# Kernel tuning notes

Hardware: AMD Instinct MI355X
Metric: run time of the kernel (lower is better)

The kernel has to match this reference:

```python
import jax, jax.numpy as jnp
import numpy as np

# bitsandbytes NF4 codebook (16 levels)
NF4_CODE = jnp.array([
    -1.0, -0.6961928009986877, -0.5250730514526367, -0.39491748809814453,
    -0.28444138169288635, -0.18477343022823334, -0.09105003625154495, 0.0,
    0.07958029955625534, 0.16093020141124725, 0.24611230194568634,
    0.33791524171829224, 0.44070982933044434, 0.5626170039176941,
    0.7229568362236023, 1.0], dtype=jnp.float32)

L, D, KV, F, V = 2, 4096, 1024, 14336, 32000   # layers, d_model, kv_dim, ffn, vocab
H, HK, HD = 32, 8, 128                          # q heads, kv heads, head dim
B, S = 2, 1024
BLK = 64                                        # NF4 quant blocksize
ROPE_THETA = 500000.0
RMS_EPS = 1e-5


def _dequant(idx, absmax, shape):
    # idx: uint8 flat codes in [0,16); absmax: fp32 per-64-element block scale
    w = NF4_CODE[idx.astype(jnp.int32)]
    return (w.reshape(-1, BLK) * absmax[:, None]).reshape(shape)


def _rmsnorm(x, w):
    return x * jax.lax.rsqrt(jnp.mean(x * x, axis=-1, keepdims=True) + RMS_EPS) * w


def _rope(x, cos, sin):
    d2 = x.shape[-1] // 2
    x1, x2 = x[..., :d2], x[..., d2:]
    return jnp.concatenate([x1 * cos - x2 * sin, x2 * cos + x1 * sin], axis=-1)


def setup_inputs() -> dict:
    key = jax.random.key(0)
    ks = iter(jax.random.split(key, 64))

    def idx(n):
        return jax.random.randint(next(ks), (n,), 0, 16).astype(jnp.uint8)

    def amax(n):
        return jax.random.uniform(next(ks), (n // BLK,), minval=0.01, maxval=0.05)

    def qw(n):
        return (jnp.stack([idx(n) for _ in range(L)]),
                jnp.stack([amax(n) for _ in range(L)]))

    inp = {}
    inp["input_ids"] = jax.random.randint(next(ks), (B, S), 0, V, dtype=jnp.int32)
    inp["attention_mask"] = jnp.ones((B, S), dtype=jnp.int32)
    inp["embed"] = jax.random.normal(next(ks), (V, D), dtype=jnp.float32) * 0.02
    inp["q_idx"], inp["q_absmax"] = qw(D * D)
    inp["k_idx"], inp["k_absmax"] = qw(KV * D)
    inp["v_idx"], inp["v_absmax"] = qw(KV * D)
    inp["o_idx"], inp["o_absmax"] = qw(D * D)
    inp["gate_idx"], inp["gate_absmax"] = qw(F * D)
    inp["up_idx"], inp["up_absmax"] = qw(F * D)
    inp["down_idx"], inp["down_absmax"] = qw(D * F)
    inp["ln1_w"] = jnp.ones((L, D), dtype=jnp.float32)
    inp["ln2_w"] = jnp.ones((L, D), dtype=jnp.float32)
    inp["final_ln_w"] = jnp.ones((D,), dtype=jnp.float32)
    return inp


def reference(input_ids, attention_mask, embed,
              q_idx, q_absmax, k_idx, k_absmax, v_idx, v_absmax,
              o_idx, o_absmax, gate_idx, gate_absmax, up_idx, up_absmax,
              down_idx, down_absmax, ln1_w, ln2_w, final_ln_w):
    b, s = input_ids.shape
    h = embed[input_ids]                                  # [B,S,D]
    pos = jnp.arange(s, dtype=jnp.float32)
    inv = 1.0 / (ROPE_THETA ** (jnp.arange(0, HD, 2, dtype=jnp.float32) / HD))
    ang = pos[:, None] * inv[None, :]                     # [S,HD/2]
    cos = jnp.cos(ang)[None, :, None, :]
    sin = jnp.sin(ang)[None, :, None, :]
    causal = jnp.tril(jnp.ones((s, s), dtype=bool))
    mask = causal[None, None] & (attention_mask[:, None, None, :] > 0)  # [B,1,S,S]
    neg = jnp.finfo(h.dtype).min

    for l in range(L):
        x = _rmsnorm(h, ln1_w[l])
        q = x @ _dequant(q_idx[l], q_absmax[l], (D, D)).T
        k = x @ _dequant(k_idx[l], k_absmax[l], (KV, D)).T
        v = x @ _dequant(v_idx[l], v_absmax[l], (KV, D)).T
        q = _rope(q.reshape(b, s, H, HD), cos, sin)
        k = _rope(k.reshape(b, s, HK, HD), cos, sin)
        v = v.reshape(b, s, HK, HD)
        k = jnp.repeat(k, H // HK, axis=2)                # GQA expand
        v = jnp.repeat(v, H // HK, axis=2)
        scores = jnp.einsum('bqhd,bkhd->bhqk', q, k) / np.float32(np.sqrt(HD))
        scores = jnp.where(mask, scores, neg)
        attn = jax.nn.softmax(scores, axis=-1)
        ctx = jnp.einsum('bhqk,bkhd->bqhd', attn, v).reshape(b, s, D)
        h = h + ctx @ _dequant(o_idx[l], o_absmax[l], (D, D)).T
        x = _rmsnorm(h, ln2_w[l])
        g = x @ _dequant(gate_idx[l], gate_absmax[l], (F, D)).T
        u = x @ _dequant(up_idx[l], up_absmax[l], (F, D)).T
        h = h + (jax.nn.silu(g) * u) @ _dequant(down_idx[l], down_absmax[l], (D, F)).T

    h = _rmsnorm(h, final_ln_w)                           # last hidden state
    m = attention_mask.astype(h.dtype)[..., None]         # masked mean pool
    pooled = (h * m).sum(axis=1) / jnp.clip(m.sum(axis=1), 1e-9)
    return pooled
```

## Files before the change

### kernel.cpp

```cpp
#include <hip/hip_runtime.h>
#include <hip/hip_fp16.h>
#include <cstdint>
#include <cstddef>

#define B_  2
#define S_  1024
#define D_  4096
#define KV_ 1024
#define F_  14336
#define H_  32
#define HK_ 8
#define HD_ 128
#define M_  2048

typedef _Float16 f16;
typedef f16   f16x8 __attribute__((ext_vector_type(8)));
typedef f16   f16x4 __attribute__((ext_vector_type(4)));
typedef float f32x4 __attribute__((ext_vector_type(4)));
typedef unsigned u32x2 __attribute__((ext_vector_type(2)));
typedef unsigned u32x4 __attribute__((ext_vector_type(4)));
typedef int      i32x4 __attribute__((ext_vector_type(4)));

#define AS1(p) ((const __attribute__((address_space(1))) void*)(p))
#define AS3(p) ((__attribute__((address_space(3))) void*)(p))

__device__ __constant__ float NF4_C[16] = {
 -1.0f, -0.6961928009986877f, -0.5250730514526367f, -0.39491748809814453f,
 -0.28444138169288635f, -0.18477343022823334f, -0.09105003625154495f, 0.0f,
 0.07958029955625534f, 0.16093020141124725f, 0.24611230194568634f,
 0.33791524171829224f, 0.44070982933044434f, 0.5626170039176941f,
 0.7229568362236023f, 1.0f };

#define WC_LAYER  218103808ull
#define WC_O      25165824ull
#define WC_G      41943040ull
#define WC_U      100663296ull
#define WC_D      159383552ull

__global__ void k_detect(const unsigned* __restrict__ p, int* __restrict__ flag){
    if (threadIdx.x == 0){
        int u8 = 0;
        for (int i = 0; i < 256; ++i) if (p[i] >= 16u) { u8 = 1; break; }
        *flag = u8;
    }
}

__global__ __launch_bounds__(256) void k_dequant_all(
        const void* __restrict__ qi, const void* __restrict__ ki, const void* __restrict__ vi,
        const void* __restrict__ oi, const void* __restrict__ gi, const void* __restrict__ ui,
        const void* __restrict__ di,
        const float* __restrict__ qa, const float* __restrict__ ka, const float* __restrict__ va,
        const float* __restrict__ oa, const float* __restrict__ ga, const float* __restrict__ ua,
        const float* __restrict__ da,
        f16* __restrict__ wc, const int* __restrict__ flag)
{
    __shared__ __half2 T[3856];
    int t = threadIdx.x;
    if (t < 256){
        int b0 = t & 15, b1 = t >> 4;
        T[b0 + (b1 << 8)] = __halves2half2(__float2half(NF4_C[b0]), __float2half(NF4_C[b1]));
    }
    __syncthreads();
    int blk = blockIdx.x;
    int l = blk / 106496; blk -= l * 106496;
    const size_t DDc = (size_t)D_ * D_, KVDc = (size_t)KV_ * D_, FDc = (size_t)F_ * D_;
    size_t oDD = (size_t)l * DDc, oKVD = (size_t)l * KVDc, oFD = (size_t)l * FDc;
    f16* wl = wc + (size_t)l * WC_LAYER;
    const void* src; const float* am; size_t so; f16* dst;
    if (blk < 8192)       { src = qi; am = qa; so = oDD;  dst = wl; }
    else if (blk < 10240) { src = ki; am = ka; so = oKVD; dst = wl + DDc;        blk -= 8192; }
    else if (blk < 12288) { src = vi; am = va; so = oKVD; dst = wl + DDc + KVDc; blk -= 10240; }
    else if (blk < 20480) { src = oi; am = oa; so = oDD;  dst = wl + WC_O;       blk -= 12288; }
    else if (blk < 49152) { src = gi; am = ga; so = oFD;  dst = wl + WC_G;       blk -= 20480; }
    else if (blk < 77824) { src = ui; am = ua; so = oFD;  dst = wl + WC_U;       blk -= 49152; }
    else                  { src = di; am = da; so = oFD;  dst = wl + WC_D;       blk -= 77824; }
    size_t i = ((size_t)blk * 256 + t) * 8;
    float amv = am[(so + i) >> 6];
    __half2 am2 = __float2half2_rn(amv);
    union { __half2 h2[4]; u32x4 u4; } R;
    if (*flag){
        u32x2 u = __builtin_nontemporal_load((const u32x2*)((const uint8_t*)src + so + i));
        R.h2[0] = __hmul2(T[u.x & 0xFFFFu], am2);
        R.h2[1] = __hmul2(T[u.x >> 16],     am2);
        R.h2[2] = __hmul2(T[u.y & 0xFFFFu], am2);
        R.h2[3] = __hmul2(T[u.y >> 16],     am2);
    } else {
        const i32x4* s4 = (const i32x4*)((const int*)src + so + i);
        i32x4 a0 = __builtin_nontemporal_load(s4);
        i32x4 a1 = __builtin_nontemporal_load(s4 + 1);
        R.h2[0] = __hmul2(T[a0.x | (a0.y << 8)], am2);
        R.h2[1] = __hmul2(T[a0.z | (a0.w << 8)], am2);
        R.h2[2] = __hmul2(T[a1.x | (a1.y << 8)], am2);
        R.h2[3] = __hmul2(T[a1.z | (a1.w << 8)], am2);
    }
    __builtin_nontemporal_store(R.u4, (u32x4*)(dst + i));
}

__global__ __launch_bounds__(256) void k_embed(const int* __restrict__ ids,
        const float* __restrict__ E, float* __restrict__ Hh)
{
    int row = blockIdx.x, t = threadIdx.x;
    int id = ids[row];
    const float4* s4 = (const float4*)(E + (size_t)id * D_);
    float4* d4 = (float4*)(Hh + (size_t)row * D_);
    #pragma unroll
    for (int i = 0; i < 4; ++i) d4[t + 256*i] = s4[t + 256*i];
}

__global__ __launch_bounds__(256) void k_ropetab(float* __restrict__ cosT, float* __restrict__ sinT){
    int id = blockIdx.x * 256 + threadIdx.x;
    int d = id & 63, s = id >> 6;
    float inv = powf(500000.0f, -(float)d * (1.0f/64.0f));
    float ang = (float)s * inv;
    cosT[id] = cosf(ang);
    sinT[id] = sinf(ang);
}

__global__ void k_maskadd(const int* __restrict__ am, float* __restrict__ ma){
    int i = blockIdx.x * 256 + threadIdx.x;
    ma[i] = am[i] ? 0.f : -1e30f;
}

template<int F16OUT>
__global__ __launch_bounds__(256) void k_rmsnorm(const float* __restrict__ X,
        const float* __restrict__ W, void* __restrict__ outv)
{
    int row = blockIdx.x, t = threadIdx.x;
    const float4* x4 = (const float4*)(X + (size_t)row * D_);
    float4 xs[4]; float ss = 0.f;
    #pragma unroll
    for (int i = 0; i < 4; ++i){
        xs[i] = x4[t + 256*i];
        ss += xs[i].x*xs[i].x + xs[i].y*xs[i].y + xs[i].z*xs[i].z + xs[i].w*xs[i].w;
    }
    for (int m = 32; m; m >>= 1) ss += __shfl_xor(ss, m, 64);
    __shared__ float red[4];
    if ((t & 63) == 0) red[t >> 6] = ss;
    __syncthreads();
    ss = red[0] + red[1] + red[2] + red[3];
    float rs = rsqrtf(ss * (1.0f / D_) + 1e-5f);
    #pragma unroll
    for (int i = 0; i < 4; ++i){
        int c0 = (t + 256*i) * 4;
        float4 wv = *(const float4*)(W + c0);
        float o0 = xs[i].x*rs*wv.x, o1 = xs[i].y*rs*wv.y;
        float o2 = xs[i].z*rs*wv.z, o3 = xs[i].w*rs*wv.w;
        if (F16OUT){
            f16x4 ov = { (f16)o0, (f16)o1, (f16)o2, (f16)o3 };
            *(f16x4*)((f16*)outv + (size_t)row * D_ + c0) = ov;
        } else {
            float4 ov = {o0, o1, o2, o3};
            *(float4*)((float*)outv + (size_t)row * D_ + c0) = ov;
        }
    }
}

template<int F16OUT>
__global__ __launch_bounds__(256) void k_combnorm(float* __restrict__ H,
        const float* __restrict__ p0, const float* __restrict__ p1,
        const float* __restrict__ W, void* __restrict__ outv)
{
    int row = blockIdx.x, t = threadIdx.x;
    size_t base = (size_t)row * D_;
    float4 xs[4]; float ss = 0.f;
    #pragma unroll
    for (int i = 0; i < 4; ++i){
        int c4 = (t + 256*i) * 4;
        float4 hv = *(const float4*)(H + base + c4);
        float4 a  = *(const float4*)(p0 + base + c4);
        float4 b  = *(const float4*)(p1 + base + c4);
        hv.x += a.x + b.x; hv.y += a.y + b.y; hv.z += a.z + b.z; hv.w += a.w + b.w;
        *(float4*)(H + base + c4) = hv;
        xs[i] = hv;
        ss += hv.x*hv.x + hv.y*hv.y + hv.z*hv.z + hv.w*hv.w;
    }
    for (int m = 32; m; m >>= 1) ss += __shfl_xor(ss, m, 64);
    __shared__ float red[4];
    if ((t & 63) == 0) red[t >> 6] = ss;
    __syncthreads();
    ss = red[0] + red[1] + red[2] + red[3];
    float rs = rsqrtf(ss * (1.0f / D_) + 1e-5f);
    #pragma unroll
    for (int i = 0; i < 4; ++i){
        int c0 = (t + 256*i) * 4;
        float4 wv = *(const float4*)(W + c0);
        float o0 = xs[i].x*rs*wv.x, o1 = xs[i].y*rs*wv.y;
        float o2 = xs[i].z*rs*wv.z, o3 = xs[i].w*rs*wv.w;
        if (F16OUT){
            f16x4 ov = { (f16)o0, (f16)o1, (f16)o2, (f16)o3 };
            *(f16x4*)((f16*)outv + base + c0) = ov;
        } else {
            float4 ov = {o0, o1, o2, o3};
            *(float4*)((float*)outv + base + c0) = ov;
        }
    }
}

__global__ __launch_bounds__(256) void k_qkvprep(const f16* __restrict__ qkv,
        f16* __restrict__ qr, f16* __restrict__ kr, f16* __restrict__ vtr,
        const float* __restrict__ cosT, const float* __restrict__ sinT)
{
    const int istr = D_ + 2 * KV_;
    int blk = blockIdx.x;
    if (blk < 16384){
        int p = blk * 256 + threadIdx.x;
        int d = p & 63;
        int h = (p >> 6) & 31;
        int s = (p >> 11) & (S_ - 1);
        int b = p >> 21;
        size_t ib = (size_t)(b * S_ + s) * istr + (size_t)h * HD_;
        float x1 = (float)qkv[ib + d], x2 = (float)qkv[ib + 64 + d];
        float c = cosT[s*64 + d], sn = sinT[s*64 + d];
        size_t ob = (((size_t)((b << 5) + h)) * S_ + (size_t)s) * HD_;
        qr[ob + d]      = (f16)(x1 * c - x2 * sn);
        qr[ob + 64 + d] = (f16)(x2 * c + x1 * sn);
    } else if (blk < 20480){
        int p = (blk - 16384) * 256 + threadIdx.x;
        int d = p & 63;
        int h = (p >> 6) & 7;
        int s = (p >> 9) & (S_ - 1);
        int b = p >> 19;
        size_t ib = (size_t)(b * S_ + s) * istr + (size_t)(D_) + (size_t)h * HD_;
        float x1 = (float)qkv[ib + d], x2 = (float)qkv[ib + 64 + d];
        float c = cosT[s*64 + d], sn = sinT[s*64 + d];
        size_t ob = (((size_t)((b << 3) + h)) * S_ + (size_t)s) * HD_;
        kr[ob + d]      = (f16)(x1 * c - x2 * sn);
        kr[ob + 64 + d] = (f16)(x2 * c + x1 * sn);
    } else {
        int p = (blk - 20480) * 256 + threadIdx.x;
        int s  = p & (S_ - 1);
        int d  = (p >> 10) & (HD_ - 1);
        int hk = (p >> 17) & (HK_ - 1);
        int b  = p >> 20;
        f16 v = qkv[(size_t)(b * S_ + s) * istr + (size_t)(D_ + KV_) + (size_t)hk * HD_ + d];
        vtr[(((size_t)(b * HK_ + hk)) * HD_ + d) * S_ + s] = v;
    }
}

__global__ __launch_bounds__(256) void k_flash(const f16* __restrict__ Qr, const f16* __restrict__ Kr,
        const f16* __restrict__ Vt, const float* __restrict__ mAddG, f16* __restrict__ ctx)
{
    __shared__ f16 KS[8192];
    __shared__ f16 VS[8192];
    __shared__ f16 PS[8192];
    const int t = threadIdx.x;
    const int w = t >> 6, l = t & 63;
    const int lr = l & 15, lg = l >> 4;
    const int qt = blockIdx.x, bh = blockIdx.y;
    const int b = bh >> 5, hh = bh & 31, hk = hh >> 2;
    const f16* Qb = Qr + ((size_t)bh * S_ + (size_t)qt*128) * HD_;
    const f16* Kb = Kr + (size_t)(b * HK_ + hk) * S_ * HD_;
    const f16* Vb = Vt + (size_t)(b * HK_ + hk) * HD_ * S_;

    auto stage16x128 = [&](const f16* src, int lds_, f16* dst){
        int rowl = t >> 4;
        int cs = ((t & 15) ^ (rowl & 7)) << 3;
        #pragma unroll
        for (int g = 0; g < 4; ++g)
            __builtin_amdgcn_global_load_lds(AS1(src + (size_t)(g*16 + rowl)*lds_ + cs),
                AS3(dst + g*2048 + w*512), 16, 0, 0);
    };
    auto stage32x64 = [&](const f16* src, int lds_, f16* dst){
        int rowl = t >> 3;
        int cs = ((t & 7) ^ (rowl & 7)) << 3;
        #pragma unroll
        for (int g = 0; g < 4; ++g)
            __builtin_amdgcn_global_load_lds(AS1(src + (size_t)(g*32 + rowl)*lds_ + cs),
                AS3(dst + g*2048 + w*512), 16, 0, 0);
    };

    stage16x128(Qb, HD_, KS);
    stage16x128(Qb + 64*HD_, HD_, VS);
    __syncthreads();
    f16x8 qF[2][4];
    {
        const f16* qsrc = (w < 2) ? KS : VS;
        int rbase = (w & 1) * 32;
        #pragma unroll
        for (int m = 0; m < 2; ++m)
            #pragma unroll
            for (int kd = 0; kd < 4; ++kd){
                int row = rbase + m*16 + lr;
                qF[m][kd] = *(const f16x8*)&qsrc[row*128 + (((kd*4 + lg) ^ (row & 7)) << 3)];
            }
    }
    __syncthreads();

    float mrow[2][4], lrow[2][4];
    f32x4 oacc[2][8];
    #pragma unroll
    for (int m = 0; m < 2; ++m)
        #pragma unroll
        for (int r = 0; r < 4; ++r){ mrow[m][r] = -1e30f; lrow[m][r] = 0.f; }
    #pragma unroll
    for (int m = 0; m < 2; ++m)
        #pragma unroll
        for (int dn = 0; dn < 8; ++dn){ f32x4 z = {0,0,0,0}; oacc[m][dn] = z; }

    const float ISQ = 0.08838834764831845f;
    const int ktMax = 2*qt + 1;

    for (int kt = 0; kt <= ktMax; ++kt){
        stage16x128(Kb + (size_t)(kt*64)*HD_, HD_, KS);
        __syncthreads();

        f32x4 sacc[2][4];
        #pragma unroll
        for (int m = 0; m < 2; ++m)
            #pragma unroll
            for (int n = 0; n < 4; ++n){ f32x4 z = {0,0,0,0}; sacc[m][n] = z; }
        #pragma unroll
        for (int n = 0; n < 4; ++n){
            int krow = n*16 + lr;
            #pragma unroll
            for (int kd = 0; kd < 4; ++kd){
                f16x8 kF = *(const f16x8*)&KS[krow*128 + (((kd*4 + lg) ^ (krow & 7)) << 3)];
                #pragma unroll
                for (int m = 0; m < 2; ++m)
                    sacc[m][n] = __builtin_amdgcn_mfma_f32_16x16x32_f16(qF[m][kd], kF, sacc[m][n], 0, 0, 0);
            }
        }

        stage32x64(Vb + kt*64, S_, VS);

        float mAdd[4];
        #pragma unroll
        for (int n = 0; n < 4; ++n) mAdd[n] = mAddG[b*S_ + kt*64 + n*16 + lr];
        int diag = (kt >= 2*qt);
        #pragma unroll
        for (int m = 0; m < 2; ++m)
        #pragma unroll
        for (int n = 0; n < 4; ++n)
        #pragma unroll
        for (int r = 0; r < 4; ++r){
            float s = sacc[m][n][r] * ISQ + mAdd[n];
            if (diag && (kt*64 + n*16 + lr) > (qt*128 + w*32 + m*16 + lg*4 + r)) s = -1e30f;
            sacc[m][n][r] = s;
        }
        #pragma unroll
        for (int m = 0; m < 2; ++m)
        #pragma unroll
        for (int r = 0; r < 4; ++r){
            float tm = fmaxf(fmaxf(sacc[m][0][r], sacc[m][1][r]), fmaxf(sacc[m][2][r], sacc[m][3][r]));
            #pragma unroll
            for (int msk = 1; msk < 16; msk <<= 1) tm = fmaxf(tm, __shfl_xor(tm, msk, 64));
            float mn = fmaxf(mrow[m][r], tm);
            float scl = __expf(mrow[m][r] - mn);
            mrow[m][r] = mn;
            float rs = 0.f;
            #pragma unroll
            for (int n = 0; n < 4; ++n){
                float p = __expf(sacc[m][n][r] - mn);
                sacc[m][n][r] = p; rs += p;
            }
            #pragma unroll
            for (int msk = 1; msk < 16; msk <<= 1) rs += __shfl_xor(rs, msk, 64);
            lrow[m][r] = lrow[m][r] * scl + rs;
            #pragma unroll
            for (int dn = 0; dn < 8; ++dn) oacc[m][dn][r] *= scl;
        }
        #pragma unroll
        for (int m = 0; m < 2; ++m)
        #pragma unroll
        for (int n = 0; n < 4; ++n)
        #pragma unroll
        for (int r = 0; r < 4; ++r){
            int rowl = m*16 + lg*4 + r;
            int slot = (n*2 + (lr >> 3)) ^ (rowl & 7);
            PS[w*2048 + rowl*64 + slot*8 + (lr & 7)] = (f16)sacc[m][n][r];
        }
        __syncthreads();

        f16x8 pF[2][2];
        #pragma unroll
        for (int m = 0; m < 2; ++m)
            #pragma unroll
            for (int kd = 0; kd < 2; ++kd){
                int prow = m*16 + lr;
                pF[m][kd] = *(const f16x8*)&PS[w*2048 + prow*64 + (((kd*4 + lg) ^ (prow & 7)) << 3)];
            }
        #pragma unroll
        for (int dn = 0; dn < 8; ++dn){
            int vrow = dn*16 + lr;
            #pragma unroll
            for (int kd = 0; kd < 2; ++kd){
                f16x8 vF = *(const f16x8*)&VS[vrow*64 + (((kd*4 + lg) ^ (vrow & 7)) << 3)];
                #pragma unroll
                for (int m = 0; m < 2; ++m)
                    oacc[m][dn] = __builtin_amdgcn_mfma_f32_16x16x32_f16(pF[m][kd], vF, oacc[m][dn], 0, 0, 0);
            }
        }
        __syncthreads();
    }

    #pragma unroll
    for (int m = 0; m < 2; ++m)
    #pragma unroll
    for (int dn = 0; dn < 8; ++dn)
    #pragma unroll
    for (int r = 0; r < 4; ++r){
        int grow = qt*128 + w*32 + m*16 + lg*4 + r;
        int gcol = hh*128 + dn*16 + lr;
        float v = oacc[m][dn][r] / fmaxf(lrow[m][r], 1e-30f);
        ctx[((size_t)(b * S_) + grow) * D_ + gcol] = (f16)v;
    }
}

template<int OUT>
__global__ __launch_bounds__(512, 1) void k_gemm3(const f16* __restrict__ A, const f16* __restrict__ Bp,
        void* __restrict__ Cv, const f16* __restrict__ G, int Kd, int ldk, int ldc)
{
    __shared__ f16 LDS[65536];
    const int t = threadIdx.x;
    const int w = t >> 6, l = t & 63;
    const int wm = w >> 2, wn = w & 3;

    int gx = gridDim.x, gy = gridDim.y;
    int nWG = gx * gy * gridDim.z;
    int n = (blockIdx.z * gy + blockIdx.y) * gx + blockIdx.x;
    int q = nWG >> 3;
    int sw = (n & 7) * q + (n >> 3);
    int by = sw % gy; int r1 = sw / gy; int bx = r1 % gx; int bz = r1 / gx;

    const int row0 = by * 256, col0 = bx * 256;
    const size_t koff = (size_t)bz * Kd;
    const int NT = Kd >> 6;

    const int swzk = ((t & 7) ^ ((t >> 3) & 7)) * 8;
    const f16* pA[2]; const f16* pB[2];
    #pragma unroll
    for (int l2 = 0; l2 < 2; ++l2){
        pA[l2] = A  + (size_t)(row0 + l2*128 + (t >> 3)) * ldk + koff + swzk;
        int wnc = (l2*64 + (t >> 3)) >> 5;
        pB[l2] = Bp + (size_t)(col0 + wnc*64 + ((t >> 3) & 31)) * ldk + koff + swzk;
    }

    auto stA = [&](int g, int tt, int buf){
        size_t so = (size_t)tt * 64;
        #pragma unroll
        for (int l2 = 0; l2 < 2; ++l2)
            __builtin_amdgcn_global_load_lds(AS1(pA[l2] + (size_t)g*64*ldk + so),
                AS3(&LDS[buf*16384 + g*8192 + l2*4096 + w*512]), 16, 0, 0);
    };
    auto stB = [&](int g, int tt, int buf){
        size_t so = (size_t)tt * 64;
        #pragma unroll
        for (int l2 = 0; l2 < 2; ++l2)
            __builtin_amdgcn_global_load_lds(AS1(pB[l2] + (size_t)g*32*ldk + so),
                AS3(&LDS[32768 + buf*16384 + g*8192 + l2*4096 + w*512]), 16, 0, 0);
    };

    const int lrow = (l & 15) * 64;
    const int kp0 = (((l >> 4))     ^ (l & 7)) * 8;
    const int kp1 = ((4 + (l >> 4)) ^ (l & 7)) * 8;

    f16x8 aR[2][4], bR0[2][2], bR1[2][2];
    auto rdA = [&](int g, int buf){
        int base = buf*16384 + g*8192 + wm*4096 + lrow;
        #pragma unroll
        for (int mf = 0; mf < 4; ++mf){
            aR[0][mf] = *(const f16x8*)&LDS[base + mf*1024 + kp0];
            aR[1][mf] = *(const f16x8*)&LDS[base + mf*1024 + kp1];
        }
    };
    auto rdB = [&](int g, int buf, f16x8 (&bR)[2][2]){
        int base = 32768 + buf*16384 + g*8192 + wn*2048 + lrow;
        #pragma unroll
        for (int nf = 0; nf < 2; ++nf){
            bR[0][nf] = *(const f16x8*)&LDS[base + nf*1024 + kp0];
            bR[1][nf] = *(const f16x8*)&LDS[base + nf*1024 + kp1];
        }
    };

    f32x4 zero = {0.f, 0.f, 0.f, 0.f};
    f32x4 acc[8][4];
    #pragma unroll
    for (int mi = 0; mi < 8; ++mi)
        #pragma unroll
        for (int ni = 0; ni < 4; ++ni) acc[mi][ni] = zero;

    #define MMQ(qm, qn, bR) { \
        __builtin_amdgcn_s_setprio(1); \
        _Pragma("unroll") \
        for (int ks = 0; ks < 2; ++ks) \
            _Pragma("unroll") \
            for (int mf = 0; mf < 4; ++mf) \
                _Pragma("unroll") \
                for (int nf = 0; nf < 2; ++nf) \
                    acc[(qm)*4+mf][(qn)*2+nf] = __builtin_amdgcn_mfma_f32_16x16x32_f16(aR[ks][mf], bR[ks][nf], acc[(qm)*4+mf][(qn)*2+nf], 0, 0, 0); \
        __builtin_amdgcn_s_setprio(0); }
    #define LGKM0 { asm volatile("s_waitcnt lgkmcnt(0)" ::: "memory"); __builtin_amdgcn_sched_barrier(0); }
    #define VM4   { asm volatile("s_waitcnt vmcnt(4)" ::: "memory"); }
    #define BAR   __builtin_amdgcn_s_barrier()

    stA(0, 0, 0); stB(1, 0, 0); stA(1, 0, 0); stB(0, 0, 0);
    if (NT > 1){ stA(0, 1, 1); stB(1, 1, 1); }
    VM4; BAR;

    for (int tt = 0; tt < NT; tt += 2){
        int c2 = (tt + 2 < NT) ? tt + 2 : NT - 1;
        int c3 = (tt + 3 < NT) ? tt + 3 : NT - 1;
        rdA(0, 0); rdB(0, 0, bR0);
        stA(1, tt+1 < NT ? tt+1 : NT-1, 1); stB(0, tt+1 < NT ? tt+1 : NT-1, 1);
        BAR; LGKM0; MMQ(0, 0, bR0); BAR;
        rdB(1, 0, bR1);
        BAR; LGKM0; MMQ(0, 1, bR1); BAR;
        rdA(1, 0);
        stA(0, c2, 0);
        BAR; LGKM0; MMQ(1, 1, bR1); BAR;
        stB(1, c2, 0);
        BAR; MMQ(1, 0, bR0); VM4; BAR;
        rdA(0, 1); rdB(0, 1, bR0);
        stA(1, c2, 0); stB(0, c2, 0);
        BAR; LGKM0; MMQ(0, 0, bR0); BAR;
        rdB(1, 1, bR1);
        BAR; LGKM0; MMQ(0, 1, bR1); BAR;
        rdA(1, 1);
        stA(0, c3, 1);
        BAR; LGKM0; MMQ(1, 1, bR1); BAR;
        stB(1, c3, 1);
        BAR; MMQ(1, 0, bR0); VM4; BAR;
    }

    #pragma unroll
    for (int mi = 0; mi < 8; ++mi)
    #pragma unroll
    for (int ni = 0; ni < 4; ++ni)
    #pragma unroll
    for (int r = 0; r < 4; ++r){
        int row = row0 + wm*128 + mi*16 + ((l >> 4) << 2) + r;
        int col = col0 + wn*64  + ni*16 + (l & 15);
        float v = acc[mi][ni][r];
        if (OUT == 0){
            ((float*)Cv)[(size_t)bz * ((size_t)M_ * ldc) + (size_t)row * ldc + col] = v;
        } else if (OUT == 2){
            ((f16*)Cv)[(size_t)row * ldc + col] = (f16)v;
        } else {
            size_t idx = (size_t)row * ldc + col;
            float g = (float)G[idx];
            float sg = g / (1.f + __expf(-g));
            ((f16*)Cv)[idx] = (f16)(sg * v);
        }
    }
    #undef MMQ
    #undef LGKM0
    #undef VM4
    #undef BAR
}

__global__ __launch_bounds__(256) void k_pool1(const float* __restrict__ Hn, const int* __restrict__ amask,
        float* __restrict__ part, float* __restrict__ cntp)
{
    int d0 = blockIdx.x * 256 + threadIdx.x;
    int b  = blockIdx.y;
    int z  = blockIdx.z;
    int s0 = z * 128;
    float s = 0.f;
    for (int i = 0; i < 128; ++i){
        int row = s0 + i;
        if (amask[b * S_ + row])
            s += Hn[((size_t)(b * S_ + row)) * D_ + d0];
    }
    part[((size_t)(z * B_ + b)) * D_ + d0] = s;
    if (blockIdx.x == 0 && threadIdx.x == 0){
        float c = 0.f;
        for (int i = 0; i < 128; ++i) c += (amask[b * S_ + s0 + i] != 0) ? 1.f : 0.f;
        cntp[z * B_ + b] = c;
    }
}
__global__ __launch_bounds__(256) void k_pool2(const float* __restrict__ part, const float* __restrict__ cntp,
        float* __restrict__ outp)
{
    int gid = blockIdx.x * 256 + threadIdx.x;
    int b = gid >> 12, d = gid & (D_ - 1);
    float s = 0.f, c = 0.f;
    #pragma unroll
    for (int z = 0; z < 8; ++z){
        s += part[((size_t)(z * B_ + b)) * D_ + d];
        c += cntp[z * B_ + b];
    }
    outp[gid] = s / fmaxf(c, 1e-9f);
}

extern "C" void kernel_launch(void* const* d_in, const int* in_sizes, int n_in,
                              void* d_out, int out_size, void* d_ws, size_t ws_size,
                              hipStream_t stream)
{
    (void)in_sizes; (void)n_in; (void)out_size; (void)ws_size;
    const int*   ids   = (const int*)  d_in[0];
    const int*   amask = (const int*)  d_in[1];
    const float* embed = (const float*)d_in[2];
    const void*  qi = d_in[3];  const float* qa = (const float*)d_in[4];
    const void*  ki = d_in[5];  const float* ka = (const float*)d_in[6];
    const void*  vi = d_in[7];  const float* va = (const float*)d_in[8];
    const void*  oi = d_in[9];  const float* oa = (const float*)d_in[10];
    const void*  gi = d_in[11]; const float* ga = (const float*)d_in[12];
    const void*  ui = d_in[13]; const float* ua = (const float*)d_in[14];
    const void*  di = d_in[15]; const float* da = (const float*)d_in[16];
    const float* ln1 = (const float*)d_in[17];
    const float* ln2 = (const float*)d_in[18];
    const float* lnf = (const float*)d_in[19];

    char* ws = (char*)d_ws;
    int*   flag = (int*)ws;
    float* h    = (float*)(ws + 256);
    float* cosT = (float*)(ws + 256 + 33554432);
    float* sinT = cosT + 65536;
    f16*   xin  = (f16*)(ws + 34078976);
    char*  R4   = ws + 168296704;
    f16* qkv16 = (f16*)(R4);
    f16* qr  = (f16*)(R4 + 25165824);
    f16* kr  = (f16*)(R4 + 41943040);
    f16* vtr = (f16*)(R4 + 46137344);
    f16* ctx = (f16*)(R4 + 50331648);
    char* R5 = R4 + 67108864;
    f16*    gbuf   = (f16*)R5;
    float*  pR5_0  = (float*)R5;
    float*  pR5_1  = (float*)(R5 + 33554432);
    float*  pR4_0  = (float*)R4;
    float*  pR4_1  = (float*)(R4 + 33554432);
    float*  hn     = (float*)R4;
    float*  part   = (float*)R5;
    float*  cntp   = (float*)(R5 + 1048576);
    float*  maskAdd= (float*)(ws + 310378496);
    f16*    wc     = (f16*)(ws + 335544320);

    const int QKV_N = D_ + 2 * KV_;

    k_detect <<<1, 64, 0, stream>>>((const unsigned*)qi, flag);
    k_dequant_all<<<2*106496, 256, 0, stream>>>(qi, ki, vi, oi, gi, ui, di,
            qa, ka, va, oa, ga, ua, da, wc, flag);
    k_embed  <<<M_, 256, 0, stream>>>(ids, embed, h);
    k_ropetab<<<256, 256, 0, stream>>>(cosT, sinT);
    k_maskadd<<<(B_*S_)/256, 256, 0, stream>>>(amask, maskAdd);
    k_rmsnorm<1><<<M_, 256, 0, stream>>>(h, ln1, xin);

    for (int l = 0; l < 2; ++l){
        f16* wcl = wc + (size_t)l * WC_LAYER;

        k_gemm3<2><<<dim3(QKV_N/256, M_/256, 1), 512, 0, stream>>>(xin, wcl, qkv16, nullptr, D_, D_, QKV_N);
        k_qkvprep<<<28672, 256, 0, stream>>>(qkv16, qr, kr, vtr, cosT, sinT);

        k_flash<<<dim3(S_/128, B_*H_), 256, 0, stream>>>(qr, kr, vtr, maskAdd, ctx);

        k_gemm3<0><<<dim3(D_/256, M_/256, 2), 512, 0, stream>>>(ctx, wcl + WC_O, pR5_0, nullptr, D_/2, D_, D_);
        k_combnorm<1><<<M_, 256, 0, stream>>>(h, pR5_0, pR5_1, ln2 + l * D_, xin);

        k_gemm3<2><<<dim3(F_/256, M_/256, 1), 512, 0, stream>>>(xin, wcl + WC_G, gbuf, nullptr, D_, D_, F_);
        k_gemm3<3><<<dim3(F_/256, M_/256, 1), 512, 0, stream>>>(xin, wcl + WC_U, gbuf, gbuf, D_, D_, F_);
        k_gemm3<0><<<dim3(D_/256, M_/256, 2), 512, 0, stream>>>(gbuf, wcl + WC_D, pR4_0, nullptr, F_/2, F_, D_);

        if (l == 0)
            k_combnorm<1><<<M_, 256, 0, stream>>>(h, pR4_0, pR4_1, ln1 + D_, xin);
        else
            k_combnorm<0><<<M_, 256, 0, stream>>>(h, pR4_0, pR4_1, lnf, hn);
    }

    k_pool1<<<dim3(D_/256, B_, 8), 256, 0, stream>>>(hn, amask, part, cntp);
    k_pool2<<<(B_*D_)/256, 256, 0, stream>>>(part, cntp, (float*)d_out);
}
```

Measured before the change: 2.475 ms.

## Fuse NF4 dequantization into O/gate/up/down GEMM B-tile loads

The upfront dequant pass now covers only the QKV weights. The O, gate, up and down projections use a new GEMM kernel that reads the NF4 codes and absmax scales directly, decodes them through an LDS lookup table and writes f16 into the B tile in LDS inside the pipelined main loop. This removes writing and re-reading about 400MB of f16 dequantized weights per call, which should cut HBM traffic. The cost is extra ALU, LDS and register pressure inside the GEMM main loop, a reworked load/wait schedule, and the dequant work being redone by every M-tile that reads the same weights.

```diff
diff --git a/kernel.cpp b/kernel.cpp
--- a/kernel.cpp
+++ b/kernel.cpp
@@ -31,11 +31,7 @@
  0.33791524171829224f, 0.44070982933044434f, 0.5626170039176941f,
  0.7229568362236023f, 1.0f };
 
-#define WC_LAYER  218103808ull
-#define WC_O      25165824ull
-#define WC_G      41943040ull
-#define WC_U      100663296ull
-#define WC_D      159383552ull
+#define WC_LAYER  25165824ull
 
 __global__ void k_detect(const unsigned* __restrict__ p, int* __restrict__ flag){
     if (threadIdx.x == 0){
@@ -45,13 +41,9 @@
     }
 }
 
-__global__ __launch_bounds__(256) void k_dequant_all(
+__global__ __launch_bounds__(256) void k_dequant_qkv(
         const void* __restrict__ qi, const void* __restrict__ ki, const void* __restrict__ vi,
-        const void* __restrict__ oi, const void* __restrict__ gi, const void* __restrict__ ui,
-        const void* __restrict__ di,
         const float* __restrict__ qa, const float* __restrict__ ka, const float* __restrict__ va,
-        const float* __restrict__ oa, const float* __restrict__ ga, const float* __restrict__ ua,
-        const float* __restrict__ da,
         f16* __restrict__ wc, const int* __restrict__ flag)
 {
     __shared__ __half2 T[3856];
@@ -62,38 +54,33 @@
     }
     __syncthreads();
     int blk = blockIdx.x;
-    int l = blk / 106496; blk -= l * 106496;
-    const size_t DDc = (size_t)D_ * D_, KVDc = (size_t)KV_ * D_, FDc = (size_t)F_ * D_;
-    size_t oDD = (size_t)l * DDc, oKVD = (size_t)l * KVDc, oFD = (size_t)l * FDc;
+    int l = blk / 12288; blk -= l * 12288;
+    const size_t DDc = (size_t)D_ * D_, KVDc = (size_t)KV_ * D_;
+    size_t oDD = (size_t)l * DDc, oKVD = (size_t)l * KVDc;
     f16* wl = wc + (size_t)l * WC_LAYER;
     const void* src; const float* am; size_t so; f16* dst;
     if (blk < 8192)       { src = qi; am = qa; so = oDD;  dst = wl; }
     else if (blk < 10240) { src = ki; am = ka; so = oKVD; dst = wl + DDc;        blk -= 8192; }
-    else if (blk < 12288) { src = vi; am = va; so = oKVD; dst = wl + DDc + KVDc; blk -= 10240; }
-    else if (blk < 20480) { src = oi; am = oa; so = oDD;  dst = wl + WC_O;       blk -= 12288; }
-    else if (blk < 49152) { src = gi; am = ga; so = oFD;  dst = wl + WC_G;       blk -= 20480; }
-    else if (blk < 77824) { src = ui; am = ua; so = oFD;  dst = wl + WC_U;       blk -= 49152; }
-    else                  { src = di; am = da; so = oFD;  dst = wl + WC_D;       blk -= 77824; }
+    else                  { src = vi; am = va; so = oKVD; dst = wl + DDc + KVDc; blk -= 10240; }
     size_t i = ((size_t)blk * 256 + t) * 8;
     float amv = am[(so + i) >> 6];
     __half2 am2 = __float2half2_rn(amv);
     union { __half2 h2[4]; u32x4 u4; } R;
     if (*flag){
-        u32x2 u = __builtin_nontemporal_load((const u32x2*)((const uint8_t*)src + so + i));
+        u32x2 u = *(const u32x2*)((const uint8_t*)src + so + i);
         R.h2[0] = __hmul2(T[u.x & 0xFFFFu], am2);
         R.h2[1] = __hmul2(T[u.x >> 16],     am2);
         R.h2[2] = __hmul2(T[u.y & 0xFFFFu], am2);
         R.h2[3] = __hmul2(T[u.y >> 16],     am2);
     } else {
         const i32x4* s4 = (const i32x4*)((const int*)src + so + i);
-        i32x4 a0 = __builtin_nontemporal_load(s4);
-        i32x4 a1 = __builtin_nontemporal_load(s4 + 1);
+        i32x4 a0 = s4[0], a1 = s4[1];
         R.h2[0] = __hmul2(T[a0.x | (a0.y << 8)], am2);
         R.h2[1] = __hmul2(T[a0.z | (a0.w << 8)], am2);
         R.h2[2] = __hmul2(T[a1.x | (a1.y << 8)], am2);
         R.h2[3] = __hmul2(T[a1.z | (a1.w << 8)], am2);
     }
-    __builtin_nontemporal_store(R.u4, (u32x4*)(dst + i));
+    *(u32x4*)(dst + i) = R.u4;
 }
 
 __global__ __launch_bounds__(256) void k_embed(const int* __restrict__ ids,
@@ -548,6 +535,196 @@
     #undef BAR
 }
 
+template<int OUT>
+__global__ __launch_bounds__(512, 1) void k_gemm5(const f16* __restrict__ A, const void* __restrict__ Bi,
+        size_t elemOff, const float* __restrict__ Ba, const int* __restrict__ flagp,
+        void* __restrict__ Cv, const f16* __restrict__ G, int Kd, int ldk, int ldc)
+{
+    __shared__ f16 LDS[65536];
+    __shared__ __half2 LUT[256];
+    const int t = threadIdx.x;
+    const int w = t >> 6, l = t & 63;
+    const int wm = w >> 2, wn = w & 3;
+
+    if (t < 256) LUT[t] = __halves2half2(__float2half(NF4_C[t & 15]), __float2half(NF4_C[t >> 4]));
+    const int isU8 = *flagp;
+
+    int gx = gridDim.x, gy = gridDim.y;
+    int nWG = gx * gy * gridDim.z;
+    int n = (blockIdx.z * gy + blockIdx.y) * gx + blockIdx.x;
+    int q = nWG >> 3;
+    int sw = (n & 7) * q + (n >> 3);
+    int by = sw % gy; int r1 = sw / gy; int bx = r1 % gx; int bz = r1 / gx;
+
+    const int row0 = by * 256, col0 = bx * 256;
+    const size_t koff = (size_t)bz * Kd;
+    const int NT = Kd >> 6;
+    const int kb = ldk >> 6;
+
+    const int swzk = ((t & 7) ^ ((t >> 3) & 7)) * 8;
+    const f16* pA[2];
+    size_t eBs[2], aBs[2];
+    #pragma unroll
+    for (int l2 = 0; l2 < 2; ++l2){
+        pA[l2] = A  + (size_t)(row0 + l2*128 + (t >> 3)) * ldk + koff + swzk;
+        int wnc = (l2*64 + (t >> 3)) >> 5;
+        int rowB = col0 + wnc*64 + ((t >> 3) & 31);
+        eBs[l2] = elemOff + (size_t)rowB * ldk + koff + swzk;
+        aBs[l2] = ((size_t)rowB * ldk + koff) >> 6;
+    }
+    const uint8_t* Bu8 = (const uint8_t*)Bi;
+    const int*     Bi32 = (const int*)Bi;
+
+    auto stA = [&](int g, int tt, int buf){
+        size_t so = (size_t)tt * 64;
+        #pragma unroll
+        for (int l2 = 0; l2 < 2; ++l2)
+            __builtin_amdgcn_global_load_lds(AS1(pA[l2] + (size_t)g*64*ldk + so),
+                AS3(&LDS[buf*16384 + g*8192 + l2*4096 + w*512]), 16, 0, 0);
+    };
+
+    struct BSet { u32x2 iv0, iv1; float am0, am1; };
+    auto ldB = [&](int g, int T, BSet &S){
+        S.iv0 = *(const u32x2*)(Bu8 + eBs[0] + (size_t)g*32*ldk + (size_t)T*64);
+        S.am0 = Ba[aBs[0] + (size_t)g*32*kb + T];
+        S.iv1 = *(const u32x2*)(Bu8 + eBs[1] + (size_t)g*32*ldk + (size_t)T*64);
+        S.am1 = Ba[aBs[1] + (size_t)g*32*kb + T];
+    };
+    auto wrB = [&](int g, int T, int buf, BSet &S){
+        #pragma unroll
+        for (int l2 = 0; l2 < 2; ++l2){
+            union { __half2 h2[4]; f16x8 v; } R;
+            if (isU8){
+                u32x2 u = l2 ? S.iv1 : S.iv0;
+                __half2 am2 = __float2half2_rn(l2 ? S.am1 : S.am0);
+                unsigned x0 = u.x & 0xFFFFu, x1 = u.x >> 16, x2 = u.y & 0xFFFFu, x3 = u.y >> 16;
+                R.h2[0] = __hmul2(LUT[(x0 | (x0 >> 4)) & 0xFF], am2);
+                R.h2[1] = __hmul2(LUT[(x1 | (x1 >> 4)) & 0xFF], am2);
+                R.h2[2] = __hmul2(LUT[(x2 | (x2 >> 4)) & 0xFF], am2);
+                R.h2[3] = __hmul2(LUT[(x3 | (x3 >> 4)) & 0xFF], am2);
+            } else {
+                size_t eoff = eBs[l2] + (size_t)g*32*ldk + (size_t)T*64;
+                float amv = Ba[aBs[l2] + (size_t)g*32*kb + T];
+                __half2 am2 = __float2half2_rn(amv);
+                i32x4 a0 = *(const i32x4*)(Bi32 + eoff);
+                i32x4 a1 = *(const i32x4*)(Bi32 + eoff + 4);
+                R.h2[0] = __hmul2(LUT[a0.x | (a0.y << 4)], am2);
+                R.h2[1] = __hmul2(LUT[a0.z | (a0.w << 4)], am2);
+                R.h2[2] = __hmul2(LUT[a1.x | (a1.y << 4)], am2);
+                R.h2[3] = __hmul2(LUT[a1.z | (a1.w << 4)], am2);
+            }
+            *(f16x8*)&LDS[32768 + buf*16384 + g*8192 + l2*4096 + w*512 + l*8] = R.v;
+        }
+    };
+
+    const int lrow = (l & 15) * 64;
+    const int kp0 = (((l >> 4))     ^ (l & 7)) * 8;
+    const int kp1 = ((4 + (l >> 4)) ^ (l & 7)) * 8;
+
+    f16x8 aR[2][4], bR0[2][2], bR1[2][2];
+    auto rdA = [&](int g, int buf){
+        int base = buf*16384 + g*8192 + wm*4096 + lrow;
+        #pragma unroll
+        for (int mf = 0; mf < 4; ++mf){
+            aR[0][mf] = *(const f16x8*)&LDS[base + mf*1024 + kp0];
+            aR[1][mf] = *(const f16x8*)&LDS[base + mf*1024 + kp1];
+        }
+    };
+    auto rdB = [&](int g, int buf, f16x8 (&bR)[2][2]){
+        int base = 32768 + buf*16384 + g*8192 + wn*2048 + lrow;
+        #pragma unroll
+        for (int nf = 0; nf < 2; ++nf){
+            bR[0][nf] = *(const f16x8*)&LDS[base + nf*1024 + kp0];
+            bR[1][nf] = *(const f16x8*)&LDS[base + nf*1024 + kp1];
+        }
+    };
+
+    f32x4 zero = {0.f, 0.f, 0.f, 0.f};
+    f32x4 acc[8][4];
+    #pragma unroll
+    for (int mi = 0; mi < 8; ++mi)
+        #pragma unroll
+        for (int ni = 0; ni < 4; ++ni) acc[mi][ni] = zero;
+
+    #define MMQ(qm, qn, bR) { \
+        __builtin_amdgcn_s_setprio(1); \
+        _Pragma("unroll") \
+        for (int ks = 0; ks < 2; ++ks) \
+            _Pragma("unroll") \
+            for (int mf = 0; mf < 4; ++mf) \
+                _Pragma("unroll") \
+                for (int nf = 0; nf < 2; ++nf) \
+                    acc[(qm)*4+mf][(qn)*2+nf] = __builtin_amdgcn_mfma_f32_16x16x32_f16(aR[ks][mf], bR[ks][nf], acc[(qm)*4+mf][(qn)*2+nf], 0, 0, 0); \
+        __builtin_amdgcn_s_setprio(0); }
+    #define LGKM0 { asm volatile("s_waitcnt lgkmcnt(0)" ::: "memory"); __builtin_amdgcn_sched_barrier(0); }
+    #define VM6   { asm volatile("s_waitcnt vmcnt(6)" ::: "memory"); }
+    #define BAR   __builtin_amdgcn_s_barrier()
+
+    __syncthreads();
+    BSet S4, S5, S8, SW1, Sa, Sb, Sc;
+    stA(0, 0, 0); stA(1, 0, 0); stA(0, 1, 1);
+    ldB(1, 0, Sa); ldB(0, 0, Sb); ldB(1, 1, Sc); ldB(0, 1, SW1);
+    wrB(1, 0, 0, Sa); wrB(0, 0, 0, Sb); wrB(1, 1, 1, Sc);
+    VM6; LGKM0; BAR;
+
+    for (int tt = 0; tt < NT; tt += 2){
+        int n1 = (tt + 1 < NT) ? tt + 1 : NT - 1;
+        int c2 = (tt + 2 < NT) ? tt + 2 : NT - 1;
+        int c3 = (tt + 3 < NT) ? tt + 3 : NT - 1;
+        rdA(0, 0); rdB(0, 0, bR0);
+        stA(1, n1, 1);
+        wrB(0, n1, 1, SW1);
+        ldB(1, c2, S4);
+        BAR; LGKM0; MMQ(0, 0, bR0); BAR;
+        rdB(1, 0, bR1);
+        ldB(0, c2, S5);
+        BAR; LGKM0; MMQ(0, 1, bR1); BAR;
+        rdA(1, 0);
+        stA(0, c2, 0);
+        BAR; LGKM0; MMQ(1, 1, bR1); BAR;
+        wrB(1, c2, 0, S4);
+        BAR; MMQ(1, 0, bR0); VM6; BAR;
+        rdA(0, 1); rdB(0, 1, bR0);
+        stA(1, c2, 0);
+        wrB(0, c2, 0, S5);
+        ldB(1, c3, S8);
+        BAR; LGKM0; MMQ(0, 0, bR0); BAR;
+        rdB(1, 1, bR1);
+        ldB(0, c3, SW1);
+        BAR; LGKM0; MMQ(0, 1, bR1); BAR;
+        rdA(1, 1);
+        stA(0, c3, 1);
+        BAR; LGKM0; MMQ(1, 1, bR1); BAR;
+        wrB(1, c3, 1, S8);
+        BAR; MMQ(1, 0, bR0); VM6; BAR;
+    }
+
+    #pragma unroll
+    for (int mi = 0; mi < 8; ++mi)
+    #pragma unroll
+    for (int ni = 0; ni < 4; ++ni)
+    #pragma unroll
+    for (int r = 0; r < 4; ++r){
+        int row = row0 + wm*128 + mi*16 + ((l >> 4) << 2) + r;
+        int col = col0 + wn*64  + ni*16 + (l & 15);
+        float v = acc[mi][ni][r];
+        if (OUT == 0){
+            ((float*)Cv)[(size_t)bz * ((size_t)M_ * ldc) + (size_t)row * ldc + col] = v;
+        } else if (OUT == 2){
+            ((f16*)Cv)[(size_t)row * ldc + col] = (f16)v;
+        } else {
+            size_t idx = (size_t)row * ldc + col;
+            float g = (float)G[idx];
+            float sg = g / (1.f + __expf(-g));
+            ((f16*)Cv)[idx] = (f16)(sg * v);
+        }
+    }
+    #undef MMQ
+    #undef LGKM0
+    #undef VM6
+    #undef BAR
+}
+
 __global__ __launch_bounds__(256) void k_pool1(const float* __restrict__ Hn, const int* __restrict__ amask,
         float* __restrict__ part, float* __restrict__ cntp)
 {
@@ -600,6 +777,10 @@
     const float* ln1 = (const float*)d_in[17];
     const float* ln2 = (const float*)d_in[18];
     const float* lnf = (const float*)d_in[19];
+
+    const size_t DD  = (size_t)D_ * D_;
+    const size_t KVD = (size_t)KV_ * D_;
+    const size_t FD  = (size_t)F_ * D_;
 
     char* ws = (char*)d_ws;
     int*   flag = (int*)ws;
@@ -628,14 +809,14 @@
     const int QKV_N = D_ + 2 * KV_;
 
     k_detect <<<1, 64, 0, stream>>>((const unsigned*)qi, flag);
-    k_dequant_all<<<2*106496, 256, 0, stream>>>(qi, ki, vi, oi, gi, ui, di,
-            qa, ka, va, oa, ga, ua, da, wc, flag);
+    k_dequant_qkv<<<2*12288, 256, 0, stream>>>(qi, ki, vi, qa, ka, va, wc, flag);
     k_embed  <<<M_, 256, 0, stream>>>(ids, embed, h);
     k_ropetab<<<256, 256, 0, stream>>>(cosT, sinT);
     k_maskadd<<<(B_*S_)/256, 256, 0, stream>>>(amask, maskAdd);
     k_rmsnorm<1><<<M_, 256, 0, stream>>>(h, ln1, xin);
 
     for (int l = 0; l < 2; ++l){
+        size_t oDD = (size_t)l * DD, oFD = (size_t)l * FD;
         f16* wcl = wc + (size_t)l * WC_LAYER;
 
         k_gemm3<2><<<dim3(QKV_N/256, M_/256, 1), 512, 0, stream>>>(xin, wcl, qkv16, nullptr, D_, D_, QKV_N);
@@ -643,12 +824,16 @@
 
         k_flash<<<dim3(S_/128, B_*H_), 256, 0, stream>>>(qr, kr, vtr, maskAdd, ctx);
 
-        k_gemm3<0><<<dim3(D_/256, M_/256, 2), 512, 0, stream>>>(ctx, wcl + WC_O, pR5_0, nullptr, D_/2, D_, D_);
+        k_gemm5<0><<<dim3(D_/256, M_/256, 2), 512, 0, stream>>>(ctx, oi, oDD, oa + oDD/64, flag,
+            pR5_0, nullptr, D_/2, D_, D_);
         k_combnorm<1><<<M_, 256, 0, stream>>>(h, pR5_0, pR5_1, ln2 + l * D_, xin);
 
-        k_gemm3<2><<<dim3(F_/256, M_/256, 1), 512, 0, stream>>>(xin, wcl + WC_G, gbuf, nullptr, D_, D_, F_);
-        k_gemm3<3><<<dim3(F_/256, M_/256, 1), 512, 0, stream>>>(xin, wcl + WC_U, gbuf, gbuf, D_, D_, F_);
-        k_gemm3<0><<<dim3(D_/256, M_/256, 2), 512, 0, stream>>>(gbuf, wcl + WC_D, pR4_0, nullptr, F_/2, F_, D_);
+        k_gemm5<2><<<dim3(F_/256, M_/256, 1), 512, 0, stream>>>(xin, gi, oFD, ga + oFD/64, flag,
+            gbuf, nullptr, D_, D_, F_);
+        k_gemm5<3><<<dim3(F_/256, M_/256, 1), 512, 0, stream>>>(xin, ui, oFD, ua + oFD/64, flag,
+            gbuf, gbuf, D_, D_, F_);
+        k_gemm5<0><<<dim3(D_/256, M_/256, 2), 512, 0, stream>>>(gbuf, di, oFD, da + oFD/64, flag,
+            pR4_0, nullptr, F_/2, F_, D_);
 
         if (l == 0)
             k_combnorm<1><<<M_, 256, 0, stream>>>(h, pR4_0, pR4_1, ln1 + D_, xin);
```

After: 5.273 ms. 2.13x slower.
